# Performance work log

Hardware: AMD Instinct MI355X
Metric: run time of the kernel (lower is better)

The kernel has to match this reference:

```python
import jax, jax.numpy as jnp
import numpy as np

N_NODES = 100000
N_EDGES = 1600000


def gcn_conv(x, W, b, src, dst, norm):
    # x: [N, Fin] -> [N, Fout]; transform-then-aggregate (GCNConv order)
    h = x @ W
    msg = h[src] * norm[:, None]            # gather + degree-normalized messages
    agg = jax.ops.segment_sum(msg, dst, num_segments=N_NODES)  # scatter-add
    return agg + b


def setup_inputs() -> dict:
    key = jax.random.key(0)
    ks = jax.random.split(key, 6)
    x = jax.random.normal(ks[0], (N_NODES, 50), dtype=jnp.float32)
    edge_index = jax.random.randint(ks[1], (2, N_EDGES), 0, N_NODES, dtype=jnp.int32)
    def glorot(k, fin, fout):
        s = jnp.sqrt(2.0 / (fin + fout)).astype(jnp.float32)
        return jax.random.normal(k, (fin, fout), dtype=jnp.float32) * s
    return {
        "x": x,
        "edge_index": edge_index,
        "W1": glorot(ks[2], 50, 128),  "b1": jnp.zeros((128,), jnp.float32),
        "W2": glorot(ks[3], 128, 128), "b2": jnp.zeros((128,), jnp.float32),
        "W3": glorot(ks[4], 128, 128), "b3": jnp.zeros((128,), jnp.float32),
        "W4": glorot(ks[5], 128, 121), "b4": jnp.zeros((121,), jnp.float32),
    }


def reference(x, edge_index, W1, b1, W2, b2, W3, b3, W4, b4):
    # GCNConv with self-loops and symmetric normalization D^-1/2 (A+I) D^-1/2
    loop = jnp.arange(N_NODES, dtype=edge_index.dtype)
    src = jnp.concatenate([edge_index[0], loop])
    dst = jnp.concatenate([edge_index[1], loop])
    deg = jax.ops.segment_sum(jnp.ones_like(dst, dtype=x.dtype), dst,
                              num_segments=N_NODES)
    dis = jnp.where(deg > 0, jax.lax.rsqrt(jnp.maximum(deg, 1e-12)), 0.0)
    norm = dis[src] * dis[dst]               # [E + N]

    h = jax.nn.relu(gcn_conv(x, W1, b1, src, dst, norm))
    h = jax.nn.relu(gcn_conv(h, W2, b2, src, dst, norm))
    h = jax.nn.relu(gcn_conv(h, W3, b3, src, dst, norm))
    out = gcn_conv(h, W4, b4, src, dst, norm)
    return jax.nn.sigmoid(out)
```

## Files before the change

### kernel.cpp

```cpp
#include <hip/hip_runtime.h>
#include <math.h>

#define NNODES 100000
#define BSHIFT 9
#define NBKT ((NNODES + (1 << BSHIFT) - 1) >> BSHIFT)
#define CAPB 10240
#define CHUNK 2048

typedef _Float16 f16x8 __attribute__((ext_vector_type(8)));
typedef _Float16 f16x2 __attribute__((ext_vector_type(2)));
typedef float f32x4 __attribute__((ext_vector_type(4)));

__global__ __launch_bounds__(256) void bin_kernel(
        const int* __restrict__ eidx, int E,
        unsigned* __restrict__ bedge, int* __restrict__ bcur) {
    __shared__ int hist[256];
    __shared__ int scanx[256];
    __shared__ int gbase[256];
    __shared__ unsigned stage[CHUNK];
    int tid = threadIdx.x;
    int base = blockIdx.x * CHUNK;
    if (base >= E) return;
    int m = min(CHUNK, E - base);
    hist[tid] = 0;
    __syncthreads();
    unsigned pk[8];
    int b[8], r[8];
#pragma unroll
    for (int j = 0; j < 8; ++j) {
        int rel = j * 256 + tid;
        bool ok = rel < m;
        int e = base + (ok ? rel : 0);
        int s = eidx[e];
        int d = eidx[E + e];
        b[j] = d >> BSHIFT;
        pk[j] = ((unsigned)(d & ((1 << BSHIFT) - 1)) << 17) | (unsigned)s;
        r[j] = ok ? atomicAdd(&hist[b[j]], 1) : -1;
    }
    __syncthreads();
    int h = hist[tid];
    scanx[tid] = h;
    __syncthreads();
    for (int st = 1; st < 256; st <<= 1) {
        int y = (tid >= st) ? scanx[tid - st] : 0;
        __syncthreads();
        scanx[tid] += y;
        __syncthreads();
    }
    int excl = scanx[tid] - h;
    if (h > 0) gbase[tid] = atomicAdd(&bcur[tid], h);
    __syncthreads();
    scanx[tid] = excl;
    __syncthreads();
#pragma unroll
    for (int j = 0; j < 8; ++j)
        if (r[j] >= 0) stage[scanx[b[j]] + r[j]] = pk[j];
    __syncthreads();
    for (int i = tid; i < m; i += 256) {
        int lo = 0, hi = NBKT - 1;
        while (lo < hi) {
            int mid = (lo + hi + 1) >> 1;
            if (scanx[mid] <= i) lo = mid; else hi = mid - 1;
        }
        int idx = gbase[lo] + (i - scanx[lo]);
        if (idx < CAPB) bedge[(size_t)lo * CAPB + idx] = stage[i];
    }
}

__global__ __launch_bounds__(512) void count2_kernel(
        const unsigned* __restrict__ bedge, const int* __restrict__ bcur,
        int* __restrict__ counts, int n) {
    __shared__ int h[512];
    int b = blockIdx.x;
    int tid = threadIdx.x;
    h[tid] = 0;
    __syncthreads();
    int cnt = min(bcur[b], CAPB);
    const unsigned* e = bedge + (size_t)b * CAPB;
    for (int i = tid; i < cnt; i += 512) atomicAdd(&h[e[i] >> 17], 1);
    __syncthreads();
    int node = b * 512 + tid;
    if (node < n) counts[node] = h[tid];
}

__global__ void dis_kernel(const int* __restrict__ counts, float* __restrict__ dis, int n) {
    int i = blockIdx.x * 256 + threadIdx.x;
    if (i < n) dis[i] = rsqrtf((float)(counts[i] + 1));
    else if (i == n) dis[i] = 0.f;
}

__global__ void scan_local(const int* __restrict__ counts, int* __restrict__ offs,
                           int* __restrict__ bsums, int n) {
    __shared__ int tsum[256];
    int t = threadIdx.x;
    int base = blockIdx.x * 1024 + t * 4;
    int v0 = (base + 0 < n) ? ((counts[base + 0] + 7) & ~7) : 0;
    int v1 = (base + 1 < n) ? ((counts[base + 1] + 7) & ~7) : 0;
    int v2 = (base + 2 < n) ? ((counts[base + 2] + 7) & ~7) : 0;
    int v3 = (base + 3 < n) ? ((counts[base + 3] + 7) & ~7) : 0;
    tsum[t] = v0 + v1 + v2 + v3;
    __syncthreads();
    for (int d = 1; d < 256; d <<= 1) {
        int x = tsum[t];
        int y = (t >= d) ? tsum[t - d] : 0;
        __syncthreads();
        tsum[t] = x + y;
        __syncthreads();
    }
    int prev = (t > 0) ? tsum[t - 1] : 0;
    if (base + 0 < n) offs[base + 0] = prev;
    if (base + 1 < n) offs[base + 1] = prev + v0;
    if (base + 2 < n) offs[base + 2] = prev + v0 + v1;
    if (base + 3 < n) offs[base + 3] = prev + v0 + v1 + v2;
    if (t == 255) bsums[blockIdx.x] = tsum[255];
}

__global__ void scan_bsums(int* __restrict__ bsums, int nb) {
    __shared__ int s[128];
    int t = threadIdx.x;
    s[t] = (t < nb) ? bsums[t] : 0;
    __syncthreads();
    for (int d = 1; d < 128; d <<= 1) {
        int x = s[t];
        int y = (t >= d) ? s[t - d] : 0;
        __syncthreads();
        s[t] = x + y;
        __syncthreads();
    }
    int excl = (t > 0) ? s[t - 1] : 0;
    if (t < nb) bsums[t] = excl;
}

__global__ void add_base(int* __restrict__ offs, const int* __restrict__ bsums, int n) {
    int i = blockIdx.x * 256 + threadIdx.x;
    if (i < n) offs[i] += bsums[i >> 10];
}

__global__ __launch_bounds__(512) void fill2_kernel(
        const unsigned* __restrict__ bedge, const int* __restrict__ bcur,
        const int* __restrict__ offs, int* __restrict__ csrc, int n) {
    __shared__ int lofs[512];
    __shared__ int lcur[512];
    int b = blockIdx.x;
    int tid = threadIdx.x;
    int node = b * 512 + tid;
    lofs[tid] = (node < n) ? offs[node] : 0;
    lcur[tid] = 0;
    __syncthreads();
    int cnt = min(bcur[b], CAPB);
    const unsigned* e = bedge + (size_t)b * CAPB;
    for (int i = tid; i < cnt; i += 512) {
        unsigned pk = e[i];
        int dl = pk >> 17;
        int p = lofs[dl] + atomicAdd(&lcur[dl], 1);
        csrc[p] = (int)(pk & 0x1FFFFu);
    }
}

__global__ void pad_kernel(const int* __restrict__ offs, const int* __restrict__ counts,
                           int* __restrict__ csrc, int n) {
    int i = blockIdx.x * 256 + threadIdx.x;
    if (i >= n) return;
    int c = counts[i];
    int p = (c + 7) & ~7;
    int o = offs[i];
    for (int j = c; j < p; ++j) csrc[o + j] = NNODES;
}

__global__ void cast_pad_kernel(const float* __restrict__ src, _Float16* __restrict__ dst,
                                int n) {
    int t = blockIdx.x * 256 + threadIdx.x;
    if (t >= n * 32) return;
    int node = t >> 5;
    int cp = t & 31;
    int c = cp * 2;
    float v0 = (c < 50) ? src[(size_t)node * 50 + c] : 0.f;
    float v1 = (c + 1 < 50) ? src[(size_t)node * 50 + c + 1] : 0.f;
    f16x2 h;
    h.x = (_Float16)v0;
    h.y = (_Float16)v1;
    *(f16x2*)&dst[(size_t)node * 64 + c] = h;
}

__global__ void wfrag_kernel(const float* __restrict__ W, f16x8* __restrict__ frag,
                             int FIN, int FOUT, int KCN, int CTN) {
    int idx = blockIdx.x * 256 + threadIdx.x;
    int tot = KCN * CTN * 64;
    if (idx >= tot) return;
    int lane = idx & 63;
    int ct = (idx >> 6) % CTN;
    int kc = (idx >> 6) / CTN;
    int c = ct * 16 + (lane & 15);
    int kb = kc * 32 + (lane >> 4) * 8;
    f16x8 v;
#pragma unroll
    for (int j = 0; j < 8; ++j) {
        int k = kb + j;
        float w = (k < FIN && c < FOUT) ? W[(size_t)k * FOUT + c] : 0.f;
        v[j] = (_Float16)w;
    }
    frag[idx] = v;
}

template <int KCN, int ACT, typename OT>
__global__ __launch_bounds__(256) void fused_kernel(
        const f16x2* __restrict__ in, const int* __restrict__ offs,
        const int* __restrict__ counts, const int* __restrict__ csrc,
        const float* __restrict__ dis, const f16x8* __restrict__ wfrag,
        const float* __restrict__ bias, int fout,
        OT* __restrict__ out, int ldo, int n) {
    constexpr int K = KCN * 32;
    constexpr int ROWB = K * 2;
    constexpr int HW = K / 2;
    __shared__ __align__(16) unsigned char sA[16 * ROWB];
    int tid = threadIdx.x;
    int wv = tid >> 6, lane = tid & 63;
    int nb = blockIdx.x * 16;
    bool act = lane < HW;

#pragma unroll 1
    for (int s = 0; s < 4; ++s) {
        int node = nb + wv * 4 + s;
        float dd = dis[node];
        float a0 = 0.f, a1 = 0.f;
        if (act) {
            f16x2 self = in[(size_t)node * HW + lane];
            a0 = dd * dd * (float)self.x;
            a1 = dd * dd * (float)self.y;
        }
        int off = offs[node];
        int pcnt = (counts[node] + 7) & ~7;
        for (int j = 0; j < pcnt; j += 8) {
            int4 s0 = *(const int4*)&csrc[off + j];
            int4 s1 = *(const int4*)&csrc[off + j + 4];
            float v0 = dis[s0.x] * dd, v1 = dis[s0.y] * dd;
            float v2 = dis[s0.z] * dd, v3 = dis[s0.w] * dd;
            float v4 = dis[s1.x] * dd, v5 = dis[s1.y] * dd;
            float v6 = dis[s1.z] * dd, v7 = dis[s1.w] * dd;
            if (act) {
                f16x2 r0 = in[(size_t)s0.x * HW + lane];
                f16x2 r1 = in[(size_t)s0.y * HW + lane];
                f16x2 r2 = in[(size_t)s0.z * HW + lane];
                f16x2 r3 = in[(size_t)s0.w * HW + lane];
                f16x2 r4 = in[(size_t)s1.x * HW + lane];
                f16x2 r5 = in[(size_t)s1.y * HW + lane];
                f16x2 r6 = in[(size_t)s1.z * HW + lane];
                f16x2 r7 = in[(size_t)s1.w * HW + lane];
                a0 = fmaf(v0, (float)r0.x, a0); a1 = fmaf(v0, (float)r0.y, a1);
                a0 = fmaf(v1, (float)r1.x, a0); a1 = fmaf(v1, (float)r1.y, a1);
                a0 = fmaf(v2, (float)r2.x, a0); a1 = fmaf(v2, (float)r2.y, a1);
                a0 = fmaf(v3, (float)r3.x, a0); a1 = fmaf(v3, (float)r3.y, a1);
                a0 = fmaf(v4, (float)r4.x, a0); a1 = fmaf(v4, (float)r4.y, a1);
                a0 = fmaf(v5, (float)r5.x, a0); a1 = fmaf(v5, (float)r5.y, a1);
                a0 = fmaf(v6, (float)r6.x, a0); a1 = fmaf(v6, (float)r6.y, a1);
                a0 = fmaf(v7, (float)r7.x, a0); a1 = fmaf(v7, (float)r7.y, a1);
            }
        }
        int r = wv * 4 + s;
        if (act) {
            f16x2 o;
            o.x = (_Float16)a0;
            o.y = (_Float16)a1;
            *(f16x2*)(sA + r * ROWB + ((lane * 4) ^ ((r & 7) << 4))) = o;
        }
    }
    __syncthreads();

    int r = lane & 15, g = lane >> 4;
    f32x4 acc[2];
    acc[0] = (f32x4){0.f, 0.f, 0.f, 0.f};
    acc[1] = (f32x4){0.f, 0.f, 0.f, 0.f};
#pragma unroll
    for (int kc = 0; kc < KCN; ++kc) {
        f16x8 a = *(const f16x8*)(sA + r * ROWB + ((kc * 64 + g * 16) ^ ((r & 7) << 4)));
        f16x8 b0 = wfrag[(size_t)(kc * 8 + wv * 2 + 0) * 64 + lane];
        f16x8 b1 = wfrag[(size_t)(kc * 8 + wv * 2 + 1) * 64 + lane];
        acc[0] = __builtin_amdgcn_mfma_f32_16x16x32_f16(a, b0, acc[0], 0, 0, 0);
        acc[1] = __builtin_amdgcn_mfma_f32_16x16x32_f16(a, b1, acc[1], 0, 0, 0);
    }
#pragma unroll
    for (int c = 0; c < 2; ++c) {
        int col = (wv * 2 + c) * 16 + r;
        if (col >= fout) continue;
        float bv = bias[col];
#pragma unroll
        for (int q = 0; q < 4; ++q) {
            int orow = nb + g * 4 + q;
            float v = acc[c][q] + bv;
            if (ACT == 0) v = fmaxf(v, 0.f);
            else v = 1.f / (1.f + __expf(-v));
            out[(size_t)orow * ldo + col] = (OT)v;
        }
    }
}

extern "C" void kernel_launch(void* const* d_in, const int* in_sizes, int n_in,
                              void* d_out, int out_size, void* d_ws, size_t ws_size,
                              hipStream_t stream) {
    const float* x = (const float*)d_in[0];
    const int* eidx = (const int*)d_in[1];
    const float* W1 = (const float*)d_in[2];
    const float* b1 = (const float*)d_in[3];
    const float* W2 = (const float*)d_in[4];
    const float* b2 = (const float*)d_in[5];
    const float* W3 = (const float*)d_in[6];
    const float* b3 = (const float*)d_in[7];
    const float* W4 = (const float*)d_in[8];
    const float* b4 = (const float*)d_in[9];
    float* out = (float*)d_out;

    const int N = NNODES;
    const int E = in_sizes[1] / 2;
    const size_t PE = (size_t)E + 8u * N;

    char* ws = (char*)d_ws;
    size_t off = 0;
    auto alloc = [&](size_t bytes) -> char* {
        char* p = ws + off;
        off = (off + bytes + 255) & ~(size_t)255;
        return p;
    };
    float* dis = (float*)alloc((size_t)(N + 1) * 4);
    int* counts = (int*)alloc((size_t)N * 4);
    int* offs = (int*)alloc((size_t)N * 4);
    int* bsums = (int*)alloc(128 * 4);
    int* bcur = (int*)alloc(256 * 4);
    int* csrc = (int*)alloc(PE * 4);
    _Float16* hA = (_Float16*)alloc((size_t)(N + 1) * 128 * 2);
    _Float16* hB = (_Float16*)alloc((size_t)(N + 1) * 128 * 2);
    _Float16* x16 = (_Float16*)alloc((size_t)(N + 1) * 64 * 2);
    f16x8* wf1 = (f16x8*)alloc((size_t)2 * 8 * 64 * 16);
    f16x8* wf2 = (f16x8*)alloc((size_t)4 * 8 * 64 * 16);
    f16x8* wf3 = (f16x8*)alloc((size_t)4 * 8 * 64 * 16);
    f16x8* wf4 = (f16x8*)alloc((size_t)4 * 8 * 64 * 16);
    unsigned* bedge = (unsigned*)hB;

    hipMemsetAsync(bcur, 0, 256 * 4, stream);

    wfrag_kernel<<<(2 * 8 * 64 + 255) / 256, 256, 0, stream>>>(W1, wf1, 50, 128, 2, 8);
    wfrag_kernel<<<(4 * 8 * 64 + 255) / 256, 256, 0, stream>>>(W2, wf2, 128, 128, 4, 8);
    wfrag_kernel<<<(4 * 8 * 64 + 255) / 256, 256, 0, stream>>>(W3, wf3, 128, 128, 4, 8);
    wfrag_kernel<<<(4 * 8 * 64 + 255) / 256, 256, 0, stream>>>(W4, wf4, 128, 121, 4, 8);

    bin_kernel<<<(E + CHUNK - 1) / CHUNK, 256, 0, stream>>>(eidx, E, bedge, bcur);
    count2_kernel<<<NBKT, 512, 0, stream>>>(bedge, bcur, counts, N);
    dis_kernel<<<(N + 256) / 256, 256, 0, stream>>>(counts, dis, N);
    int nb = (N + 1023) / 1024;
    scan_local<<<nb, 256, 0, stream>>>(counts, offs, bsums, N);
    scan_bsums<<<1, 128, 0, stream>>>(bsums, nb);
    add_base<<<(N + 255) / 256, 256, 0, stream>>>(offs, bsums, N);
    fill2_kernel<<<NBKT, 512, 0, stream>>>(bedge, bcur, offs, csrc, N);
    pad_kernel<<<(N + 255) / 256, 256, 0, stream>>>(offs, counts, csrc, N);

    cast_pad_kernel<<<(N * 32 + 255) / 256, 256, 0, stream>>>(x, x16, N);

    int fblocks = N / 16;
    fused_kernel<2, 0, _Float16><<<fblocks, 256, 0, stream>>>(
        (const f16x2*)x16, offs, counts, csrc, dis, wf1, b1, 128, hA, 128, N);
    fused_kernel<4, 0, _Float16><<<fblocks, 256, 0, stream>>>(
        (const f16x2*)hA, offs, counts, csrc, dis, wf2, b2, 128, hB, 128, N);
    fused_kernel<4, 0, _Float16><<<fblocks, 256, 0, stream>>>(
        (const f16x2*)hB, offs, counts, csrc, dis, wf3, b3, 128, hA, 128, N);
    fused_kernel<4, 1, float><<<fblocks, 256, 0, stream>>>(
        (const f16x2*)hA, offs, counts, csrc, dis, wf4, b4, 121, out, 121, N);
}
```

Before: 378.3 us.

## Give each wave its own 16-node tile and drop block-wide barrier

Each wave now aggregates 16 nodes into a private shared-memory tile and computes all 8 output column tiles with MFMA itself, so the block-level __syncthreads is gone and waves run independently. Blocks now cover 64 nodes with bounds checks for the tail. A small kernel zeroes the dummy padding row (index N) of the feature buffers used by padded neighbor entries. The cost is more weight-fragment loads per wave (8 column tiles instead of 2) and more accumulator registers.

```diff
diff --git a/kernel.cpp b/kernel.cpp
--- a/kernel.cpp
+++ b/kernel.cpp
@@ -165,6 +165,14 @@
     int p = (c + 7) & ~7;
     int o = offs[i];
     for (int j = c; j < p; ++j) csrc[o + j] = NNODES;
+}
+
+__global__ void zdum_kernel(_Float16* __restrict__ x16, _Float16* __restrict__ hA,
+                            _Float16* __restrict__ hB, int n) {
+    int t = threadIdx.x;
+    if (t < 64) x16[(size_t)n * 64 + t] = (_Float16)0.f;
+    else if (t < 192) hA[(size_t)n * 128 + (t - 64)] = (_Float16)0.f;
+    else if (t < 320) hB[(size_t)n * 128 + (t - 192)] = (_Float16)0.f;
 }
 
 __global__ void cast_pad_kernel(const float* __restrict__ src, _Float16* __restrict__ dst,
@@ -212,84 +220,88 @@
     constexpr int K = KCN * 32;
     constexpr int ROWB = K * 2;
     constexpr int HW = K / 2;
-    __shared__ __align__(16) unsigned char sA[16 * ROWB];
+    __shared__ __align__(16) unsigned char sA[4][16 * ROWB];
     int tid = threadIdx.x;
     int wv = tid >> 6, lane = tid & 63;
-    int nb = blockIdx.x * 16;
+    int wnb = blockIdx.x * 64 + wv * 16;
+    if (wnb >= n) return;
+    unsigned char* tile = sA[wv];
     bool act = lane < HW;
 
 #pragma unroll 1
-    for (int s = 0; s < 4; ++s) {
-        int node = nb + wv * 4 + s;
-        float dd = dis[node];
+    for (int s = 0; s < 16; ++s) {
+        int node = wnb + s;
         float a0 = 0.f, a1 = 0.f;
-        if (act) {
-            f16x2 self = in[(size_t)node * HW + lane];
-            a0 = dd * dd * (float)self.x;
-            a1 = dd * dd * (float)self.y;
-        }
-        int off = offs[node];
-        int pcnt = (counts[node] + 7) & ~7;
-        for (int j = 0; j < pcnt; j += 8) {
-            int4 s0 = *(const int4*)&csrc[off + j];
-            int4 s1 = *(const int4*)&csrc[off + j + 4];
-            float v0 = dis[s0.x] * dd, v1 = dis[s0.y] * dd;
-            float v2 = dis[s0.z] * dd, v3 = dis[s0.w] * dd;
-            float v4 = dis[s1.x] * dd, v5 = dis[s1.y] * dd;
-            float v6 = dis[s1.z] * dd, v7 = dis[s1.w] * dd;
+        if (node < n) {
+            float dd = dis[node];
             if (act) {
-                f16x2 r0 = in[(size_t)s0.x * HW + lane];
-                f16x2 r1 = in[(size_t)s0.y * HW + lane];
-                f16x2 r2 = in[(size_t)s0.z * HW + lane];
-                f16x2 r3 = in[(size_t)s0.w * HW + lane];
-                f16x2 r4 = in[(size_t)s1.x * HW + lane];
-                f16x2 r5 = in[(size_t)s1.y * HW + lane];
-                f16x2 r6 = in[(size_t)s1.z * HW + lane];
-                f16x2 r7 = in[(size_t)s1.w * HW + lane];
-                a0 = fmaf(v0, (float)r0.x, a0); a1 = fmaf(v0, (float)r0.y, a1);
-                a0 = fmaf(v1, (float)r1.x, a0); a1 = fmaf(v1, (float)r1.y, a1);
-                a0 = fmaf(v2, (float)r2.x, a0); a1 = fmaf(v2, (float)r2.y, a1);
-                a0 = fmaf(v3, (float)r3.x, a0); a1 = fmaf(v3, (float)r3.y, a1);
-                a0 = fmaf(v4, (float)r4.x, a0); a1 = fmaf(v4, (float)r4.y, a1);
-                a0 = fmaf(v5, (float)r5.x, a0); a1 = fmaf(v5, (float)r5.y, a1);
-                a0 = fmaf(v6, (float)r6.x, a0); a1 = fmaf(v6, (float)r6.y, a1);
-                a0 = fmaf(v7, (float)r7.x, a0); a1 = fmaf(v7, (float)r7.y, a1);
+                f16x2 self = in[(size_t)node * HW + lane];
+                a0 = dd * dd * (float)self.x;
+                a1 = dd * dd * (float)self.y;
             }
-        }
-        int r = wv * 4 + s;
+            int off = offs[node];
+            int pcnt = (counts[node] + 7) & ~7;
+            for (int j = 0; j < pcnt; j += 8) {
+                int4 s0 = *(const int4*)&csrc[off + j];
+                int4 s1 = *(const int4*)&csrc[off + j + 4];
+                float v0 = dis[s0.x] * dd, v1 = dis[s0.y] * dd;
+                float v2 = dis[s0.z] * dd, v3 = dis[s0.w] * dd;
+                float v4 = dis[s1.x] * dd, v5 = dis[s1.y] * dd;
+                float v6 = dis[s1.z] * dd, v7 = dis[s1.w] * dd;
+                if (act) {
+                    f16x2 r0 = in[(size_t)s0.x * HW + lane];
+                    f16x2 r1 = in[(size_t)s0.y * HW + lane];
+                    f16x2 r2 = in[(size_t)s0.z * HW + lane];
+                    f16x2 r3 = in[(size_t)s0.w * HW + lane];
+                    f16x2 r4 = in[(size_t)s1.x * HW + lane];
+                    f16x2 r5 = in[(size_t)s1.y * HW + lane];
+                    f16x2 r6 = in[(size_t)s1.z * HW + lane];
+                    f16x2 r7 = in[(size_t)s1.w * HW + lane];
+                    a0 = fmaf(v0, (float)r0.x, a0); a1 = fmaf(v0, (float)r0.y, a1);
+                    a0 = fmaf(v1, (float)r1.x, a0); a1 = fmaf(v1, (float)r1.y, a1);
+                    a0 = fmaf(v2, (float)r2.x, a0); a1 = fmaf(v2, (float)r2.y, a1);
+                    a0 = fmaf(v3, (float)r3.x, a0); a1 = fmaf(v3, (float)r3.y, a1);
+                    a0 = fmaf(v4, (float)r4.x, a0); a1 = fmaf(v4, (float)r4.y, a1);
+                    a0 = fmaf(v5, (float)r5.x, a0); a1 = fmaf(v5, (float)r5.y, a1);
+                    a0 = fmaf(v6, (float)r6.x, a0); a1 = fmaf(v6, (float)r6.y, a1);
+                    a0 = fmaf(v7, (float)r7.x, a0); a1 = fmaf(v7, (float)r7.y, a1);
+                }
+            }
+        }
         if (act) {
             f16x2 o;
             o.x = (_Float16)a0;
             o.y = (_Float16)a1;
-            *(f16x2*)(sA + r * ROWB + ((lane * 4) ^ ((r & 7) << 4))) = o;
-        }
-    }
-    __syncthreads();
+            *(f16x2*)(tile + s * ROWB + ((lane * 4) ^ ((s & 7) << 4))) = o;
+        }
+    }
 
     int r = lane & 15, g = lane >> 4;
-    f32x4 acc[2];
-    acc[0] = (f32x4){0.f, 0.f, 0.f, 0.f};
-    acc[1] = (f32x4){0.f, 0.f, 0.f, 0.f};
+    f32x4 acc[8];
+#pragma unroll
+    for (int ct = 0; ct < 8; ++ct) acc[ct] = (f32x4){0.f, 0.f, 0.f, 0.f};
 #pragma unroll
     for (int kc = 0; kc < KCN; ++kc) {
-        f16x8 a = *(const f16x8*)(sA + r * ROWB + ((kc * 64 + g * 16) ^ ((r & 7) << 4)));
-        f16x8 b0 = wfrag[(size_t)(kc * 8 + wv * 2 + 0) * 64 + lane];
-        f16x8 b1 = wfrag[(size_t)(kc * 8 + wv * 2 + 1) * 64 + lane];
-        acc[0] = __builtin_amdgcn_mfma_f32_16x16x32_f16(a, b0, acc[0], 0, 0, 0);
-        acc[1] = __builtin_amdgcn_mfma_f32_16x16x32_f16(a, b1, acc[1], 0, 0, 0);
-    }
-#pragma unroll
-    for (int c = 0; c < 2; ++c) {
-        int col = (wv * 2 + c) * 16 + r;
+        f16x8 a = *(const f16x8*)(tile + r * ROWB + ((kc * 64 + g * 16) ^ ((r & 7) << 4)));
+#pragma unroll
+        for (int ct = 0; ct < 8; ++ct) {
+            f16x8 b = wfrag[(size_t)(kc * 8 + ct) * 64 + lane];
+            acc[ct] = __builtin_amdgcn_mfma_f32_16x16x32_f16(a, b, acc[ct], 0, 0, 0);
+        }
+    }
+#pragma unroll
+    for (int ct = 0; ct < 8; ++ct) {
+        int col = ct * 16 + r;
         if (col >= fout) continue;
         float bv = bias[col];
 #pragma unroll
         for (int q = 0; q < 4; ++q) {
-            int orow = nb + g * 4 + q;
-            float v = acc[c][q] + bv;
+            int node = wnb + g * 4 + q;
+            if (node >= n) continue;
+            float v = acc[ct][q] + bv;
             if (ACT == 0) v = fmaxf(v, 0.f);
             else v = 1.f / (1.f + __expf(-v));
-            out[(size_t)orow * ldo + col] = (OT)v;
+            out[(size_t)node * ldo + col] = (OT)v;
         }
     }
 }
@@ -351,10 +363,11 @@
     add_base<<<(N + 255) / 256, 256, 0, stream>>>(offs, bsums, N);
     fill2_kernel<<<NBKT, 512, 0, stream>>>(bedge, bcur, offs, csrc, N);
     pad_kernel<<<(N + 255) / 256, 256, 0, stream>>>(offs, counts, csrc, N);
+    zdum_kernel<<<1, 320, 0, stream>>>(x16, hA, hB, N);
 
     cast_pad_kernel<<<(N * 32 + 255) / 256, 256, 0, stream>>>(x, x16, N);
 
-    int fblocks = N / 16;
+    int fblocks = (N + 63) / 64;
     fused_kernel<2, 0, _Float16><<<fblocks, 256, 0, stream>>>(
         (const f16x2*)x16, offs, counts, csrc, dis, wf1, b1, 128, hA, 128, N);
     fused_kernel<4, 0, _Float16><<<fblocks, 256, 0, stream>>>(
```

Result: slower. 527.0 us (+39.3%).

## Interleave gathers for four nodes per wave to raise memory-level parallelism

Applied to the files above, without the earlier changes.

The fused aggregation kernel now processes a wave's four nodes together, issuing the index and row gathers for all four in each iteration instead of walking one node at a time. Nodes that run out of neighbors are masked by zeroing their weight and reading a valid index. A dummy zero row at index N is written into the feature buffers so padded indices read zeros, and launch bounds now request four blocks per SIMD. This aims to hide gather latency with more outstanding loads, at the cost of higher register pressure and wasted loads when degrees are uneven.

```diff
diff --git a/kernel.cpp b/kernel.cpp
--- a/kernel.cpp
+++ b/kernel.cpp
@@ -165,6 +165,14 @@
     int p = (c + 7) & ~7;
     int o = offs[i];
     for (int j = c; j < p; ++j) csrc[o + j] = NNODES;
+}
+
+__global__ void zdum_kernel(_Float16* __restrict__ x16, _Float16* __restrict__ hA,
+                            _Float16* __restrict__ hB, int n) {
+    int t = threadIdx.x;
+    if (t < 64) x16[(size_t)n * 64 + t] = (_Float16)0.f;
+    else if (t < 192) hA[(size_t)n * 128 + (t - 64)] = (_Float16)0.f;
+    else if (t < 320) hB[(size_t)n * 128 + (t - 192)] = (_Float16)0.f;
 }
 
 __global__ void cast_pad_kernel(const float* __restrict__ src, _Float16* __restrict__ dst,
@@ -203,7 +211,7 @@
 }
 
 template <int KCN, int ACT, typename OT>
-__global__ __launch_bounds__(256) void fused_kernel(
+__global__ __launch_bounds__(256, 4) void fused_kernel(
         const f16x2* __restrict__ in, const int* __restrict__ offs,
         const int* __restrict__ counts, const int* __restrict__ csrc,
         const float* __restrict__ dis, const f16x8* __restrict__ wfrag,
@@ -217,50 +225,70 @@
     int wv = tid >> 6, lane = tid & 63;
     int nb = blockIdx.x * 16;
     bool act = lane < HW;
-
-#pragma unroll 1
-    for (int s = 0; s < 4; ++s) {
-        int node = nb + wv * 4 + s;
-        float dd = dis[node];
-        float a0 = 0.f, a1 = 0.f;
+    int n0 = nb + wv * 4;
+
+    float dd[4], ax[4], ay[4];
+    int off[4], pc[4];
+#pragma unroll
+    for (int k = 0; k < 4; ++k) {
+        dd[k] = dis[n0 + k];
+        off[k] = offs[n0 + k];
+        pc[k] = (counts[n0 + k] + 7) & ~7;
+        ax[k] = 0.f;
+        ay[k] = 0.f;
         if (act) {
-            f16x2 self = in[(size_t)node * HW + lane];
-            a0 = dd * dd * (float)self.x;
-            a1 = dd * dd * (float)self.y;
-        }
-        int off = offs[node];
-        int pcnt = (counts[node] + 7) & ~7;
-        for (int j = 0; j < pcnt; j += 8) {
-            int4 s0 = *(const int4*)&csrc[off + j];
-            int4 s1 = *(const int4*)&csrc[off + j + 4];
-            float v0 = dis[s0.x] * dd, v1 = dis[s0.y] * dd;
-            float v2 = dis[s0.z] * dd, v3 = dis[s0.w] * dd;
-            float v4 = dis[s1.x] * dd, v5 = dis[s1.y] * dd;
-            float v6 = dis[s1.z] * dd, v7 = dis[s1.w] * dd;
+            f16x2 sv = in[(size_t)(n0 + k) * HW + lane];
+            ax[k] = dd[k] * dd[k] * (float)sv.x;
+            ay[k] = dd[k] * dd[k] * (float)sv.y;
+        }
+    }
+    int pmax = max(max(pc[0], pc[1]), max(pc[2], pc[3]));
+
+    for (int j = 0; j < pmax; j += 8) {
+        int4 i0[4], i1[4];
+        float m[4];
+#pragma unroll
+        for (int k = 0; k < 4; ++k) {
+            bool g = j < pc[k];
+            int b = off[k] + (g ? j : 0);
+            m[k] = g ? dd[k] : 0.f;
+            i0[k] = *(const int4*)&csrc[b];
+            i1[k] = *(const int4*)&csrc[b + 4];
+        }
+#pragma unroll
+        for (int k = 0; k < 4; ++k) {
+            float u0 = dis[i0[k].x] * m[k], u1 = dis[i0[k].y] * m[k];
+            float u2 = dis[i0[k].z] * m[k], u3 = dis[i0[k].w] * m[k];
+            float u4 = dis[i1[k].x] * m[k], u5 = dis[i1[k].y] * m[k];
+            float u6 = dis[i1[k].z] * m[k], u7 = dis[i1[k].w] * m[k];
             if (act) {
-                f16x2 r0 = in[(size_t)s0.x * HW + lane];
-                f16x2 r1 = in[(size_t)s0.y * HW + lane];
-                f16x2 r2 = in[(size_t)s0.z * HW + lane];
-                f16x2 r3 = in[(size_t)s0.w * HW + lane];
-                f16x2 r4 = in[(size_t)s1.x * HW + lane];
-                f16x2 r5 = in[(size_t)s1.y * HW + lane];
-                f16x2 r6 = in[(size_t)s1.z * HW + lane];
-                f16x2 r7 = in[(size_t)s1.w * HW + lane];
-                a0 = fmaf(v0, (float)r0.x, a0); a1 = fmaf(v0, (float)r0.y, a1);
-                a0 = fmaf(v1, (float)r1.x, a0); a1 = fmaf(v1, (float)r1.y, a1);
-                a0 = fmaf(v2, (float)r2.x, a0); a1 = fmaf(v2, (float)r2.y, a1);
-                a0 = fmaf(v3, (float)r3.x, a0); a1 = fmaf(v3, (float)r3.y, a1);
-                a0 = fmaf(v4, (float)r4.x, a0); a1 = fmaf(v4, (float)r4.y, a1);
-                a0 = fmaf(v5, (float)r5.x, a0); a1 = fmaf(v5, (float)r5.y, a1);
-                a0 = fmaf(v6, (float)r6.x, a0); a1 = fmaf(v6, (float)r6.y, a1);
-                a0 = fmaf(v7, (float)r7.x, a0); a1 = fmaf(v7, (float)r7.y, a1);
+                f16x2 r0 = in[(size_t)i0[k].x * HW + lane];
+                f16x2 r1 = in[(size_t)i0[k].y * HW + lane];
+                f16x2 r2 = in[(size_t)i0[k].z * HW + lane];
+                f16x2 r3 = in[(size_t)i0[k].w * HW + lane];
+                f16x2 r4 = in[(size_t)i1[k].x * HW + lane];
+                f16x2 r5 = in[(size_t)i1[k].y * HW + lane];
+                f16x2 r6 = in[(size_t)i1[k].z * HW + lane];
+                f16x2 r7 = in[(size_t)i1[k].w * HW + lane];
+                ax[k] = fmaf(u0, (float)r0.x, ax[k]); ay[k] = fmaf(u0, (float)r0.y, ay[k]);
+                ax[k] = fmaf(u1, (float)r1.x, ax[k]); ay[k] = fmaf(u1, (float)r1.y, ay[k]);
+                ax[k] = fmaf(u2, (float)r2.x, ax[k]); ay[k] = fmaf(u2, (float)r2.y, ay[k]);
+                ax[k] = fmaf(u3, (float)r3.x, ax[k]); ay[k] = fmaf(u3, (float)r3.y, ay[k]);
+                ax[k] = fmaf(u4, (float)r4.x, ax[k]); ay[k] = fmaf(u4, (float)r4.y, ay[k]);
+                ax[k] = fmaf(u5, (float)r5.x, ax[k]); ay[k] = fmaf(u5, (float)r5.y, ay[k]);
+                ax[k] = fmaf(u6, (float)r6.x, ax[k]); ay[k] = fmaf(u6, (float)r6.y, ay[k]);
+                ax[k] = fmaf(u7, (float)r7.x, ax[k]); ay[k] = fmaf(u7, (float)r7.y, ay[k]);
             }
         }
-        int r = wv * 4 + s;
-        if (act) {
+    }
+
+    if (act) {
+#pragma unroll
+        for (int k = 0; k < 4; ++k) {
+            int r = wv * 4 + k;
             f16x2 o;
-            o.x = (_Float16)a0;
-            o.y = (_Float16)a1;
+            o.x = (_Float16)ax[k];
+            o.y = (_Float16)ay[k];
             *(f16x2*)(sA + r * ROWB + ((lane * 4) ^ ((r & 7) << 4))) = o;
         }
     }
@@ -351,6 +379,7 @@
     add_base<<<(N + 255) / 256, 256, 0, stream>>>(offs, bsums, N);
     fill2_kernel<<<NBKT, 512, 0, stream>>>(bedge, bcur, offs, csrc, N);
     pad_kernel<<<(N + 255) / 256, 256, 0, stream>>>(offs, counts, csrc, N);
+    zdum_kernel<<<1, 320, 0, stream>>>(x16, hA, hB, N);
 
     cast_pad_kernel<<<(N * 32 + 255) / 256, 256, 0, stream>>>(x, x16, N);
 
```

Result: slower. 530.2 us (+40.1%).
